# Kernel optimization log

Hardware: AMD Instinct MI355X
Metric: run time of the kernel (lower is better)

## Reference

```python
import jax, jax.numpy as jnp
import numpy as np

N = 100000           # nodes
E = 1600000          # edges (no self loops; added inside reference)
IN_DIM = 128
H1, C1 = 8, 16       # layer-1 heads, per-head channels (concat -> 128)
H2, C2 = 1, 40       # layer-2 heads, out channels (concat=False)


def setup_inputs() -> dict:
    key = jax.random.key(0)
    ks = jax.random.split(key, 10)
    x = jax.random.normal(ks[0], (N, IN_DIM), jnp.float32)
    src = jax.random.randint(ks[1], (E,), 0, N, dtype=jnp.int32)
    dst = jax.random.randint(ks[2], (E,), 0, N, dtype=jnp.int32)
    dst = jnp.where(dst == src, (dst + 1) % N, dst)  # emulate remove_self_loops
    edge_index = jnp.stack([src, dst], axis=0)
    sc = 0.05
    return {
        "x": x,
        "edge_index": edge_index,
        "W1": jax.random.normal(ks[3], (H1 * C1, IN_DIM), jnp.float32) * sc,
        "b1": jnp.zeros((H1 * C1,), jnp.float32),
        "att1": jax.random.normal(ks[4], (H1, 2 * C1), jnp.float32) * sc,
        "bias1": jnp.zeros((H1 * C1,), jnp.float32),
        "W2": jax.random.normal(ks[5], (H2 * C2, H1 * C1), jnp.float32) * sc,
        "b2": jnp.zeros((H2 * C2,), jnp.float32),
        "att2": jax.random.normal(ks[6], (H2, 2 * C2), jnp.float32) * sc,
        "bias2": jnp.zeros((C2,), jnp.float32),
    }


def _gat_layer(x, src, dst, W, b, att, bias, H, C, concat):
    n = x.shape[0]
    # add self loops (inputs are guaranteed self-loop free)
    loop = jnp.arange(n, dtype=src.dtype)
    s = jnp.concatenate([src, loop])
    d = jnp.concatenate([dst, loop])
    h = (x @ W.T + b).reshape(n, H, C)            # [N,H,C]
    # per-node halves of cat([x_i, x_j]) . att  -> gather scalars per edge
    a_i = jnp.einsum('nhc,hc->nh', h, att[:, :C])  # dst half
    a_j = jnp.einsum('nhc,hc->nh', h, att[:, C:])  # src half
    e = jax.nn.leaky_relu(a_i[d] + a_j[s], negative_slope=0.2)  # [Etot,H]
    # segment softmax over destination nodes (pyg_utils.softmax)
    m = jax.ops.segment_max(e, d, num_segments=n)
    ex = jnp.exp(e - m[d])
    denom = jax.ops.segment_sum(ex, d, num_segments=n)
    alpha = ex / (denom[d] + 1e-16)
    msg = h[s] * alpha[:, :, None]                # [Etot,H,C]
    out = jax.ops.segment_sum(msg.reshape(-1, H * C), d, num_segments=n)
    if not concat:
        out = out.reshape(n, H, C).mean(axis=1)
    return out + bias


def reference(x, edge_index, W1, b1, att1, bias1, W2, b2, att2, bias2):
    src, dst = edge_index[0], edge_index[1]
    h = _gat_layer(x, src, dst, W1, b1, att1, bias1, H1, C1, True)
    h = jax.nn.elu(h)  # dropout p=0 / eval -> no-op
    h = _gat_layer(h, src, dst, W2, b2, att2, bias2, H2, C2, False)
    return jax.nn.log_softmax(h, axis=1)
```

## Files before the change

### kernel.cpp

```cpp
#include <hip/hip_runtime.h>
#include <hip/hip_fp16.h>
#include <math.h>


typedef _Float16 f16x8 __attribute__((ext_vector_type(8)));
typedef float f32x4 __attribute__((ext_vector_type(4)));
typedef float f32x2 __attribute__((ext_vector_type(2)));

__device__ __forceinline__ float lrelu02(float x){ return x > 0.f ? x : 0.2f*x; }
__device__ __forceinline__ unsigned char f2fp8(float v){
  return (unsigned char)(__builtin_amdgcn_cvt_pk_fp8_f32(v, v, 0, false) & 0xff);
}

#define BSHIFT 8
#define BMASK  255
#define SPLIT_CHUNK 4096

__device__ __forceinline__ void split_body(int blk, const int* __restrict__ src,
    const int* __restrict__ dst, int* __restrict__ hp, int* __restrict__ tmp,
    int E, int nb1){
  __shared__ int hist[512];
  __shared__ int hoff[512];
  __shared__ int sb[256];
  int tid = threadIdx.x;
  #pragma unroll
  for (int t = tid; t < 512; t += 256) hist[t] = 0;
  __syncthreads();
  int lo = blk*SPLIT_CHUNK;
  int ds[16], ss[16];
  #pragma unroll
  for (int k = 0; k < 16; ++k){
    int i = lo + tid + k*256;
    bool p = i < E;
    ds[k] = p ? dst[i] : 0;
    ss[k] = p ? src[i] : 0;
    if (p) atomicAdd(&hist[ds[k] >> BSHIFT], 1);
  }
  __syncthreads();
  int v0 = hist[2*tid], v1 = hist[2*tid+1];
  sb[tid] = v0 + v1;
  __syncthreads();
  for (int off = 1; off < 256; off <<= 1){
    int x = (tid >= off) ? sb[tid-off] : 0;
    __syncthreads();
    sb[tid] += x;
    __syncthreads();
  }
  int base = (tid == 0) ? 0 : sb[tid-1];
  hoff[2*tid]   = base;
  hoff[2*tid+1] = base + v0;
  __syncthreads();
  for (int b = tid; b < nb1; b += 256) hp[blk*nb1 + b] = hoff[b];
  __syncthreads();
  #pragma unroll
  for (int k = 0; k < 16; ++k){
    int i = lo + tid + k*256;
    if (i < E){
      int r = atomicAdd(&hoff[ds[k] >> BSHIFT], 1);
      tmp[blk*SPLIT_CHUNK + r] = ss[k] | ((ds[k] & BMASK) << 17);
    }
  }
}

__device__ __forceinline__ void gemm1_body(int gb, const float* __restrict__ x,
    const _Float16* __restrict__ Wh, const _Float16* __restrict__ attB,
    const float* __restrict__ b1, const float* __restrict__ consts,
    unsigned char* __restrict__ h1f8, float* __restrict__ a1i, float* __restrict__ a1j, int N){
  int wid  = (gb*256 + (int)threadIdx.x) >> 6;
  int lane = threadIdx.x & 63;
  int m0 = wid*16;
  if (m0 >= N) return;
  int col = lane & 15, quad = lane >> 4;
  const float* xr = x + (size_t)(m0+col)*128 + quad*8;
  f32x4 acc[9];
  #pragma unroll
  for (int t=0;t<9;t++){ acc[t][0]=0.f; acc[t][1]=0.f; acc[t][2]=0.f; acc[t][3]=0.f; }
  #pragma unroll
  for (int q=0;q<4;q++){
    float4 f0 = ((const float4*)(xr + q*32))[0];
    float4 f1 = ((const float4*)(xr + q*32))[1];
    f16x8 a;
    a[0]=(_Float16)f0.x; a[1]=(_Float16)f0.y; a[2]=(_Float16)f0.z; a[3]=(_Float16)f0.w;
    a[4]=(_Float16)f1.x; a[5]=(_Float16)f1.y; a[6]=(_Float16)f1.z; a[7]=(_Float16)f1.w;
    #pragma unroll
    for (int t=0;t<8;t++){
      const f16x8* Bp = (const f16x8*)(Wh + (size_t)(t*16+col)*128 + q*32 + quad*8);
      acc[t] = __builtin_amdgcn_mfma_f32_16x16x32_f16(a, *Bp, acc[t], 0,0,0);
    }
    const f16x8* Ap = (const f16x8*)(attB + (size_t)col*128 + q*32 + quad*8);
    acc[8] = __builtin_amdgcn_mfma_f32_16x16x32_f16(a, *Ap, acc[8], 0,0,0);
  }
  #pragma unroll
  for (int t=0;t<8;t++){
    int c = t*16 + col;
    float bb = b1[c];
    #pragma unroll
    for (int r=0;r<4;r++){
      h1f8[(size_t)(m0 + quad*4 + r)*128 + c] = f2fp8(acc[t][r] + bb);
    }
  }
  float hb = consts[col];
  #pragma unroll
  for (int r=0;r<4;r++){
    int node = m0 + quad*4 + r;
    float v = acc[8][r] + hb;
    if (col < 8) a1i[node*8 + col] = v;
    else         a1j[node*8 + (col-8)] = v;
  }
}

__global__ __launch_bounds__(256) void k_fused1(const int* __restrict__ src,
    const int* __restrict__ dst, int* __restrict__ hp, int* __restrict__ tmp,
    int E, int nb1, int nchunk,
    const float* __restrict__ x, const _Float16* __restrict__ Wh,
    const _Float16* __restrict__ attB, const float* __restrict__ b1,
    const float* __restrict__ consts, unsigned char* __restrict__ h1f8,
    float* __restrict__ a1i, float* __restrict__ a1j, int N){
  if ((int)blockIdx.x < nchunk)
    split_body(blockIdx.x, src, dst, hp, tmp, E, nb1);
  else
    gemm1_body(blockIdx.x - nchunk, x, Wh, attB, b1, consts, h1f8, a1i, a1j, N);
}

__global__ __launch_bounds__(256) void k_colsum(const int* __restrict__ hp,
    int* __restrict__ tot, int nchunk, int nb1){
  __shared__ int red[256];
  int b = blockIdx.x;
  int t = threadIdx.x;
  int s = 0;
  for (int blk = t; blk < nchunk; blk += 256)
    s += hp[blk*nb1 + b + 1] - hp[blk*nb1 + b];
  red[t] = s;
  __syncthreads();
  for (int off = 128; off > 0; off >>= 1){
    if (t < off) red[t] += red[t+off];
    __syncthreads();
  }
  if (t == 0) tot[b] = red[0];
}

__global__ void k_bscan(const int* __restrict__ tot, int* __restrict__ bstart,
                        int* __restrict__ rowstart, int nbucket, int E, int N){
  __shared__ int lds[256];
  int t = threadIdx.x;
  int v[4]; int s = 0;
  #pragma unroll
  for (int k = 0; k < 4; ++k){
    int idx = t*4 + k;
    v[k] = (idx < nbucket) ? tot[idx] : 0;
    s += v[k];
  }
  lds[t] = s;
  __syncthreads();
  for (int off = 1; off < 256; off <<= 1){
    int x = (t >= off) ? lds[t-off] : 0;
    __syncthreads();
    lds[t] += x;
    __syncthreads();
  }
  int run = (t == 0) ? 0 : lds[t-1];
  #pragma unroll
  for (int k = 0; k < 4; ++k){
    int idx = t*4 + k;
    if (idx < nbucket) bstart[idx] = run;
    run += v[k];
  }
  if (t == 0){ bstart[nbucket] = E; rowstart[N] = E; }
}

#define STAGE_CAP 6144
__global__ __launch_bounds__(256) void k_final(const int* __restrict__ tmp,
    const int* __restrict__ hp, const int* __restrict__ bstart,
    int* __restrict__ rowstart, int* __restrict__ csr, int nchunk, int nb1, int N){
  __shared__ int stage[STAGE_CAP];
  __shared__ int c0[512];
  __shared__ int cv[512];
  __shared__ int ce[512];
  __shared__ int sb[256];
  __shared__ int h[256];
  __shared__ int sc[256];
  __shared__ int cur[256];
  int b = blockIdx.x;
  int tid = threadIdx.x;
  int base = bstart[b];
  int tot  = bstart[b+1] - base;
  #pragma unroll
  for (int t = tid; t < 512; t += 256){ c0[t] = 0; cv[t] = 0; }
  __syncthreads();
  for (int blk = tid; blk < nchunk; blk += 256){
    int o0 = hp[blk*nb1 + b];
    int o1 = hp[blk*nb1 + b + 1];
    c0[blk] = o0;
    cv[blk] = o1 - o0;
  }
  __syncthreads();
  int v0 = cv[2*tid], v1 = cv[2*tid+1];
  sb[tid] = v0 + v1;
  __syncthreads();
  for (int off = 1; off < 256; off <<= 1){
    int x = (tid >= off) ? sb[tid-off] : 0;
    __syncthreads();
    sb[tid] += x;
    __syncthreads();
  }
  int pbase = (tid == 0) ? 0 : sb[tid-1];
  ce[2*tid]   = pbase;
  ce[2*tid+1] = pbase + v0;
  __syncthreads();
  for (int blk = tid; blk < nchunk; blk += 256){
    int cnt = cv[blk];
    int out = ce[blk];
    const int* tb = tmp + blk*SPLIT_CHUNK + c0[blk];
    for (int j = 0; j < cnt; ++j){
      int o = out + j;
      if (o < STAGE_CAP) stage[o] = tb[j];
    }
  }
  if (tid < 256) h[tid] = 0;
  __syncthreads();
  if (tot > STAGE_CAP) tot = STAGE_CAP;
  for (int i = tid; i < tot; i += 256) atomicAdd(&h[stage[i] >> 17], 1);
  __syncthreads();
  sc[tid] = h[tid];
  __syncthreads();
  for (int off = 1; off < 256; off <<= 1){
    int x = (tid >= off) ? sc[tid-off] : 0;
    __syncthreads();
    sc[tid] += x;
    __syncthreads();
  }
  {
    int excl = sc[tid] - h[tid];
    int node = b*256 + tid;
    if (node < N) rowstart[node] = base + excl;
    cur[tid] = excl;
  }
  __syncthreads();
  for (int i = tid; i < tot; i += 256){
    int v = stage[i];
    int p = atomicAdd(&cur[v >> 17], 1);
    csr[base + p] = v & 0x1FFFF;
  }
}

__global__ void k_prep(const float* __restrict__ W1, const float* __restrict__ b1,
                       const float* __restrict__ att1,
                       const float* __restrict__ W2, const float* __restrict__ b2,
                       const float* __restrict__ att2,
                       _Float16* __restrict__ W1h, _Float16* __restrict__ W2h,
                       _Float16* __restrict__ attB1, _Float16* __restrict__ attB2,
                       float* __restrict__ consts){
  int i = blockIdx.x*blockDim.x + threadIdx.x;
  if (i < 16384){ W1h[i] = (_Float16)W1[i]; return; }
  i -= 16384;
  if (i < 6144){ int r = i >> 7; W2h[i] = (r < 40)? (_Float16)W2[i] : (_Float16)0.f; return; }
  i -= 6144;
  if (i < 2048){
    int j = i >> 7, k = i & 127;
    int h = j & 7, half = (j >> 3)*16;
    float s = 0.f;
    for (int c = 0; c < 16; ++c) s += att1[h*32 + half + c]*W1[(h*16+c)*128 + k];
    attB1[i] = (_Float16)s; return;
  }
  i -= 2048;
  if (i < 2048){
    int j = i >> 7, k = i & 127;
    float s = 0.f;
    if (j < 2){ const float* av = att2 + j*40; for (int c = 0; c < 40; ++c) s += av[c]*W2[c*128 + k]; }
    attB2[i] = (_Float16)s; return;
  }
  i -= 2048;
  if (i < 18){
    float s = 0.f;
    if (i < 8){ for (int c = 0; c < 16; ++c) s += b1[i*16+c]*att1[i*32+c]; }
    else if (i < 16){ int h = i-8; for (int c = 0; c < 16; ++c) s += b1[h*16+c]*att1[h*32+16+c]; }
    else if (i == 16){ for (int c = 0; c < 40; ++c) s += b2[c]*att2[c]; }
    else { for (int c = 0; c < 40; ++c) s += b2[c]*att2[40+c]; }
    consts[i] = s;
  }
}

__global__ __launch_bounds__(256) void k_agg1(const uint2* __restrict__ h1q,
    const float* __restrict__ a1i, const float* __restrict__ a1j,
    const int* __restrict__ rowstart, const int* __restrict__ csr,
    const float* __restrict__ bias, uint4* __restrict__ x2u4, int N){
  int lane = threadIdx.x & 63;
  int n = (blockIdx.x*blockDim.x + threadIdx.x) >> 6;
  if (n >= N) return;
  int ql = lane & 15, qt = lane >> 4;
  unsigned hd = (unsigned)ql >> 1;
  int rs = rowstart[n], re = rowstart[n+1];
  float ai2 = a1i[(unsigned)n*8u + hd];
  float a0=0.f,a1=0.f,a2=0.f,a3=0.f,a4=0.f,a5=0.f,a6=0.f,a7=0.f,den=0.f;
  {
    float w = (qt==0)? __expf(lrelu02(ai2 + a1j[(unsigned)n*8u + hd])) : 0.f;
    uint2 u = h1q[(unsigned)n*16u + (unsigned)ql];
    f32x2 f0 = __builtin_amdgcn_cvt_pk_f32_fp8((int)u.x, false);
    f32x2 f1 = __builtin_amdgcn_cvt_pk_f32_fp8((int)u.x, true);
    f32x2 f2 = __builtin_amdgcn_cvt_pk_f32_fp8((int)u.y, false);
    f32x2 f3 = __builtin_amdgcn_cvt_pk_f32_fp8((int)u.y, true);
    a0=w*f0[0]; a1=w*f0[1]; a2=w*f1[0]; a3=w*f1[1];
    a4=w*f2[0]; a5=w*f2[1]; a6=w*f3[0]; a7=w*f3[1];
    den = w;
  }
  int last = re - 1;
  if (rs < re){
    unsigned cs0 = (unsigned)csr[min(rs+ 0+qt,last)];
    unsigned cs1 = (unsigned)csr[min(rs+ 4+qt,last)];
    unsigned cs2 = (unsigned)csr[min(rs+ 8+qt,last)];
    unsigned cs3 = (unsigned)csr[min(rs+12+qt,last)];
    unsigned cs4 = (unsigned)csr[min(rs+16+qt,last)];
    unsigned cs5 = (unsigned)csr[min(rs+20+qt,last)];
    unsigned cs6 = (unsigned)csr[min(rs+24+qt,last)];
    unsigned cs7 = (unsigned)csr[min(rs+28+qt,last)];
    float aj0 = a1j[cs0*8u+hd], aj1 = a1j[cs1*8u+hd];
    float aj2 = a1j[cs2*8u+hd], aj3 = a1j[cs3*8u+hd];
    float aj4 = a1j[cs4*8u+hd], aj5 = a1j[cs5*8u+hd];
    float aj6 = a1j[cs6*8u+hd], aj7 = a1j[cs7*8u+hd];
    uint2 u0 = h1q[(size_t)cs0*16u + (unsigned)ql];
    uint2 u1 = h1q[(size_t)cs1*16u + (unsigned)ql];
    uint2 u2 = h1q[(size_t)cs2*16u + (unsigned)ql];
    uint2 u3 = h1q[(size_t)cs3*16u + (unsigned)ql];
    int e0 = rs;

#define AGG1_ST(US, CF, CS, AJ, OFF)                                         \
    {                                                                        \
      uint2 cur = US;                                                        \
      US = h1q[(size_t)CF*16u + (unsigned)ql];                               \
      unsigned nc = (unsigned)csr[min(e0+OFF+32+qt, last)];                  \
      float w = (e0+OFF+qt < re)? __expf(lrelu02(ai2 + AJ)) : 0.f;           \
      den += w;                                                              \
      f32x2 g0 = __builtin_amdgcn_cvt_pk_f32_fp8((int)cur.x, false);         \
      f32x2 g1 = __builtin_amdgcn_cvt_pk_f32_fp8((int)cur.x, true);          \
      f32x2 g2 = __builtin_amdgcn_cvt_pk_f32_fp8((int)cur.y, false);         \
      f32x2 g3 = __builtin_amdgcn_cvt_pk_f32_fp8((int)cur.y, true);          \
      a0 += w*g0[0]; a1 += w*g0[1]; a2 += w*g1[0]; a3 += w*g1[1];            \
      a4 += w*g2[0]; a5 += w*g2[1]; a6 += w*g3[0]; a7 += w*g3[1];            \
      CS = nc; AJ = a1j[nc*8u + hd];                                         \
    }

    while (e0 < re){
      AGG1_ST(u0, cs4, cs0, aj0, 0)
      if (e0+4 >= re) break;
      AGG1_ST(u1, cs5, cs1, aj1, 4)
      if (e0+8 >= re) break;
      AGG1_ST(u2, cs6, cs2, aj2, 8)
      if (e0+12 >= re) break;
      AGG1_ST(u3, cs7, cs3, aj3, 12)
      if (e0+16 >= re) break;
      AGG1_ST(u0, cs0, cs4, aj4, 16)
      if (e0+20 >= re) break;
      AGG1_ST(u1, cs1, cs5, aj5, 20)
      if (e0+24 >= re) break;
      AGG1_ST(u2, cs2, cs6, aj6, 24)
      if (e0+28 >= re) break;
      AGG1_ST(u3, cs3, cs7, aj7, 28)
      e0 += 32;
    }
#undef AGG1_ST
  }
  #pragma unroll
  for (int off = 16; off < 64; off <<= 1){
    den += __shfl_xor(den, off);
    a0 += __shfl_xor(a0, off); a1 += __shfl_xor(a1, off);
    a2 += __shfl_xor(a2, off); a3 += __shfl_xor(a3, off);
    a4 += __shfl_xor(a4, off); a5 += __shfl_xor(a5, off);
    a6 += __shfl_xor(a6, off); a7 += __shfl_xor(a7, off);
  }
  if (qt == 0){
    float invd = 1.f/(den + 1e-16f);
    const float4* b4 = (const float4*)(bias + 8*ql);
    float4 bl = b4[0], bh = b4[1];
    float o0=a0*invd+bl.x, o1=a1*invd+bl.y, o2=a2*invd+bl.z, o3=a3*invd+bl.w;
    float o4=a4*invd+bh.x, o5=a5*invd+bh.y, o6=a6*invd+bh.z, o7=a7*invd+bh.w;
    o0=(o0>0.f)?o0:(__expf(o0)-1.f); o1=(o1>0.f)?o1:(__expf(o1)-1.f);
    o2=(o2>0.f)?o2:(__expf(o2)-1.f); o3=(o3>0.f)?o3:(__expf(o3)-1.f);
    o4=(o4>0.f)?o4:(__expf(o4)-1.f); o5=(o5>0.f)?o5:(__expf(o5)-1.f);
    o6=(o6>0.f)?o6:(__expf(o6)-1.f); o7=(o7>0.f)?o7:(__expf(o7)-1.f);
    __half2 p0 = __floats2half2_rn(o0,o1), p1 = __floats2half2_rn(o2,o3);
    __half2 p2 = __floats2half2_rn(o4,o5), p3 = __floats2half2_rn(o6,o7);
    uint4 o;
    o.x = *(unsigned*)&p0; o.y = *(unsigned*)&p1; o.z = *(unsigned*)&p2; o.w = *(unsigned*)&p3;
    x2u4[(unsigned)n*16u + (unsigned)ql] = o;
  }
}

__global__ __launch_bounds__(256) void k_gemm2(const _Float16* __restrict__ xh,
    const _Float16* __restrict__ Wh, const _Float16* __restrict__ attB,
    const float* __restrict__ b2, const float* __restrict__ consts,
    unsigned char* __restrict__ h2f8, float* __restrict__ a2i, float* __restrict__ a2j, int N){
  int wid  = (blockIdx.x*256 + threadIdx.x) >> 6;
  int lane = threadIdx.x & 63;
  int m0 = wid*16;
  if (m0 >= N) return;
  int col = lane & 15, quad = lane >> 4;
  const f16x8* A8 = (const f16x8*)(xh + (size_t)(m0+col)*128 + quad*8);
  f32x4 acc[4];
  #pragma unroll
  for (int t=0;t<4;t++){ acc[t][0]=0.f; acc[t][1]=0.f; acc[t][2]=0.f; acc[t][3]=0.f; }
  #pragma unroll
  for (int q=0;q<4;q++){
    f16x8 a = A8[q*4];
    #pragma unroll
    for (int t=0;t<3;t++){
      const f16x8* Bp = (const f16x8*)(Wh + (size_t)(t*16+col)*128 + q*32 + quad*8);
      acc[t] = __builtin_amdgcn_mfma_f32_16x16x32_f16(a, *Bp, acc[t], 0,0,0);
    }
    const f16x8* Bp2 = (const f16x8*)(attB + (size_t)col*128 + q*32 + quad*8);
    acc[3] = __builtin_amdgcn_mfma_f32_16x16x32_f16(a, *Bp2, acc[3], 0,0,0);
  }
  #pragma unroll
  for (int t=0;t<3;t++){
    int c = t*16 + col;
    if (c < 40){
      float bb = b2[c];
      #pragma unroll
      for (int r=0;r<4;r++){
        h2f8[(size_t)(m0 + quad*4 + r)*40 + c] = f2fp8(acc[t][r] + bb);
      }
    }
  }
  if (col < 2){
    float cc = consts[16 + col];
    #pragma unroll
    for (int r=0;r<4;r++){
      int node = m0 + quad*4 + r;
      if (col == 0) a2i[node] = acc[3][r] + cc;
      else          a2j[node] = acc[3][r] + cc;
    }
  }
}

__global__ __launch_bounds__(256) void k_agg2(const unsigned* __restrict__ h2u,
    const float* __restrict__ a2i, const float* __restrict__ a2j,
    const int* __restrict__ rowstart, const int* __restrict__ csr,
    const float* __restrict__ bias, float* __restrict__ out, int N){
  int lane = threadIdx.x & 63;
  int wid = (blockIdx.x*blockDim.x + threadIdx.x) >> 6;
  int qt = lane >> 4, ql = lane & 15;
  int n = wid*4 + qt;
  if (n >= N) return;
  bool act = ql < 10;
  unsigned cl = act ? (unsigned)ql : 0u;
  int rs = rowstart[n], re = rowstart[n+1];
  float ai = a2i[n];
  float wself = __expf(lrelu02(ai + a2j[n]));
  float a0,a1,a2,a3,den;
  {
    unsigned u = h2u[(unsigned)n*10u + cl];
    f32x2 f0 = __builtin_amdgcn_cvt_pk_f32_fp8((int)u, false);
    f32x2 f1 = __builtin_amdgcn_cvt_pk_f32_fp8((int)u, true);
    a0 = wself*f0[0]; a1 = wself*f0[1]; a2 = wself*f1[0]; a3 = wself*f1[1];
    den = wself;
  }
  if (rs < re){
    int last = re - 1;
    unsigned cs0 = (unsigned)csr[min(rs+0,last)];
    unsigned cs1 = (unsigned)csr[min(rs+1,last)];
    unsigned cs2 = (unsigned)csr[min(rs+2,last)];
    unsigned cs3 = (unsigned)csr[min(rs+3,last)];
    unsigned cs4 = (unsigned)csr[min(rs+4,last)];
    unsigned cs5 = (unsigned)csr[min(rs+5,last)];
    unsigned cs6 = (unsigned)csr[min(rs+6,last)];
    unsigned cs7 = (unsigned)csr[min(rs+7,last)];
    float aj0 = a2j[cs0], aj1 = a2j[cs1], aj2 = a2j[cs2], aj3 = a2j[cs3];
    float aj4 = a2j[cs4], aj5 = a2j[cs5], aj6 = a2j[cs6], aj7 = a2j[cs7];
    unsigned u0 = h2u[cs0*10u + cl];
    unsigned u1 = h2u[cs1*10u + cl];
    unsigned u2 = h2u[cs2*10u + cl];
    unsigned u3 = h2u[cs3*10u + cl];
    int e0 = rs;

#define AGG2_ST(US, CF, CS, AJ, OFF)                                         \
    {                                                                        \
      unsigned cur = US;                                                     \
      US = h2u[CF*10u + cl];                                                 \
      unsigned nc = (unsigned)csr[min(e0+OFF+8, last)];                      \
      float w = (e0+OFF < re)? __expf(lrelu02(ai + AJ)) : 0.f;               \
      den += w;                                                              \
      f32x2 g0 = __builtin_amdgcn_cvt_pk_f32_fp8((int)cur, false);           \
      f32x2 g1 = __builtin_amdgcn_cvt_pk_f32_fp8((int)cur, true);            \
      a0 += w*g0[0]; a1 += w*g0[1]; a2 += w*g1[0]; a3 += w*g1[1];            \
      CS = nc; AJ = a2j[nc];                                                 \
    }

    while (e0 < re){
      AGG2_ST(u0, cs4, cs0, aj0, 0)
      AGG2_ST(u1, cs5, cs1, aj1, 1)
      AGG2_ST(u2, cs6, cs2, aj2, 2)
      AGG2_ST(u3, cs7, cs3, aj3, 3)
      AGG2_ST(u0, cs0, cs4, aj4, 4)
      AGG2_ST(u1, cs1, cs5, aj5, 5)
      AGG2_ST(u2, cs2, cs6, aj6, 6)
      AGG2_ST(u3, cs3, cs7, aj7, 7)
      e0 += 8;
    }
#undef AGG2_ST
  }
  float invd = 1.f/(den + 1e-16f);
  const float4* b4 = (const float4*)(bias + 4*cl);
  float4 bb = b4[0];
  float v0 = a0*invd + bb.x, v1 = a1*invd + bb.y;
  float v2 = a2*invd + bb.z, v3 = a3*invd + bb.w;
  float mv = act ? fmaxf(fmaxf(v0,v1), fmaxf(v2,v3)) : -INFINITY;
  #pragma unroll
  for (int off = 1; off < 16; off <<= 1) mv = fmaxf(mv, __shfl_xor(mv, off));
  float se = act ? (__expf(v0-mv)+__expf(v1-mv)+__expf(v2-mv)+__expf(v3-mv)) : 0.f;
  #pragma unroll
  for (int off = 1; off < 16; off <<= 1) se += __shfl_xor(se, off);
  float ls = __logf(se);
  if (act){
    float4 o = make_float4(v0-mv-ls, v1-mv-ls, v2-mv-ls, v3-mv-ls);
    ((float4*)out)[(unsigned)n*10u + cl] = o;
  }
}

extern "C" void kernel_launch(void* const* d_in, const int* in_sizes, int n_in,
                              void* d_out, int out_size, void* d_ws, size_t ws_size,
                              hipStream_t stream){
  const float* x     = (const float*)d_in[0];
  const int*   ei    = (const int*)  d_in[1];
  const float* W1    = (const float*)d_in[2];
  const float* b1    = (const float*)d_in[3];
  const float* att1  = (const float*)d_in[4];
  const float* bias1 = (const float*)d_in[5];
  const float* W2    = (const float*)d_in[6];
  const float* b2    = (const float*)d_in[7];
  const float* att2  = (const float*)d_in[8];
  const float* bias2 = (const float*)d_in[9];
  int N = in_sizes[0] / 128;
  int E = in_sizes[1] / 2;
  const int* src = ei;
  const int* dst = ei + E;

  char* ws = (char*)d_ws;
  size_t off = 0;
  auto alloc = [&](size_t bytes)->char*{
    char* p = ws + off; off += (bytes + 255) & ~(size_t)255; return p;
  };
  unsigned char* h1f8 = (unsigned char*)alloc((size_t)N*128);
  _Float16*      x2h  = (_Float16*)alloc((size_t)N*128*2);
  unsigned char* h2f8 = (unsigned char*)alloc((size_t)N*40);
  float* a1i  = (float*)alloc((size_t)N*8*4);
  float* a1j  = (float*)alloc((size_t)N*8*4);
  float* a2i  = (float*)alloc((size_t)N*4);
  float* a2j  = (float*)alloc((size_t)N*4);
  _Float16* W1h   = (_Float16*)alloc(16384*2);
  _Float16* W2h   = (_Float16*)alloc(6144*2);
  _Float16* attB1 = (_Float16*)alloc(2048*2);
  _Float16* attB2 = (_Float16*)alloc(2048*2);
  float* consts = (float*)alloc(18*4);
  int*   rowst = (int*)  alloc((size_t)(N+1)*4);
  int*   csr   = (int*)  alloc((size_t)E*4);

  int nbucket = (N + BMASK) >> BSHIFT;
  int nb1 = nbucket + 1;
  int nchunk = (E + SPLIT_CHUNK - 1)/SPLIT_CHUNK;

  int*   hp     = (int*)alloc((size_t)nchunk*nb1*4);
  int*   tot    = (int*)alloc((size_t)nbucket*4);
  int*   bstart = (int*)alloc((size_t)(nbucket+1)*4);
  int*   tmp    = (int*)x2h;

  int gblk = ((N+15)/16 + 3)/4;

  k_prep<<<105, 256, 0, stream>>>(W1, b1, att1, W2, b2, att2, W1h, W2h, attB1, attB2, consts);
  k_fused1<<<nchunk + gblk, 256, 0, stream>>>(src, dst, hp, tmp, E, nb1, nchunk,
                                              x, W1h, attB1, b1, consts, h1f8, a1i, a1j, N);
  k_colsum<<<nbucket, 256, 0, stream>>>(hp, tot, nchunk, nb1);
  k_bscan<<<1, 256, 0, stream>>>(tot, bstart, rowst, nbucket, E, N);
  k_final<<<nbucket, 256, 0, stream>>>(tmp, hp, bstart, rowst, csr, nchunk, nb1, N);

  k_agg1<<<(N*64+255)/256, 256, 0, stream>>>((const uint2*)h1f8, a1i, a1j, rowst, csr, bias1, (uint4*)x2h, N);

  k_gemm2<<<gblk, 256, 0, stream>>>(x2h, W2h, attB2, b2, consts, h2f8, a2i, a2j, N);
  k_agg2<<<(N+15)/16, 256, 0, stream>>>((const unsigned*)h2f8, a2i, a2j, rowst, csr, bias2, (float*)d_out, N);
}
```

Baseline: 290.9 us.

## Fuse layer-2 GEMM into layer-1 aggregation via shared-memory tile

The layer-1 aggregation kernel now runs 16 waves per 1024-thread block, one node per wave, and stages the ELU'd fp16 outputs in shared memory. After a barrier, four waves run the layer-2 MFMA projection and attention dot products directly from that tile. This drops the separate GEMM launch and the round trip of the N×128 fp16 intermediate through global memory. In exchange it adds a block-wide sync that makes fast waves wait on the slowest-degree node, uses large blocks that may limit occupancy, and gives the temp buffer its own allocation.

```diff
diff --git a/kernel.cpp b/kernel.cpp
--- a/kernel.cpp
+++ b/kernel.cpp
@@ -280,153 +280,153 @@
   }
 }
 
-__global__ __launch_bounds__(256) void k_agg1(const uint2* __restrict__ h1q,
+__global__ __launch_bounds__(1024) void k_agg1(const uint2* __restrict__ h1q,
     const float* __restrict__ a1i, const float* __restrict__ a1j,
     const int* __restrict__ rowstart, const int* __restrict__ csr,
-    const float* __restrict__ bias, uint4* __restrict__ x2u4, int N){
-  int lane = threadIdx.x & 63;
-  int n = (blockIdx.x*blockDim.x + threadIdx.x) >> 6;
-  if (n >= N) return;
+    const float* __restrict__ bias,
+    const _Float16* __restrict__ W2h, const _Float16* __restrict__ attB2,
+    const float* __restrict__ b2, const float* __restrict__ consts,
+    unsigned char* __restrict__ h2f8, float* __restrict__ a2i, float* __restrict__ a2j,
+    int N){
+  __shared__ uint4 xt4[16][16];
+  int tid = threadIdx.x;
+  int w = tid >> 6, lane = tid & 63;
+  int m0 = blockIdx.x*16;
+  int n = m0 + w;
   int ql = lane & 15, qt = lane >> 4;
-  unsigned hd = (unsigned)ql >> 1;
-  int rs = rowstart[n], re = rowstart[n+1];
-  float ai2 = a1i[(unsigned)n*8u + hd];
-  float a0=0.f,a1=0.f,a2=0.f,a3=0.f,a4=0.f,a5=0.f,a6=0.f,a7=0.f,den=0.f;
-  {
-    float w = (qt==0)? __expf(lrelu02(ai2 + a1j[(unsigned)n*8u + hd])) : 0.f;
-    uint2 u = h1q[(unsigned)n*16u + (unsigned)ql];
-    f32x2 f0 = __builtin_amdgcn_cvt_pk_f32_fp8((int)u.x, false);
-    f32x2 f1 = __builtin_amdgcn_cvt_pk_f32_fp8((int)u.x, true);
-    f32x2 f2 = __builtin_amdgcn_cvt_pk_f32_fp8((int)u.y, false);
-    f32x2 f3 = __builtin_amdgcn_cvt_pk_f32_fp8((int)u.y, true);
-    a0=w*f0[0]; a1=w*f0[1]; a2=w*f1[0]; a3=w*f1[1];
-    a4=w*f2[0]; a5=w*f2[1]; a6=w*f3[0]; a7=w*f3[1];
-    den = w;
-  }
-  int last = re - 1;
-  if (rs < re){
-    unsigned cs0 = (unsigned)csr[min(rs+ 0+qt,last)];
-    unsigned cs1 = (unsigned)csr[min(rs+ 4+qt,last)];
-    unsigned cs2 = (unsigned)csr[min(rs+ 8+qt,last)];
-    unsigned cs3 = (unsigned)csr[min(rs+12+qt,last)];
-    unsigned cs4 = (unsigned)csr[min(rs+16+qt,last)];
-    unsigned cs5 = (unsigned)csr[min(rs+20+qt,last)];
-    unsigned cs6 = (unsigned)csr[min(rs+24+qt,last)];
-    unsigned cs7 = (unsigned)csr[min(rs+28+qt,last)];
-    float aj0 = a1j[cs0*8u+hd], aj1 = a1j[cs1*8u+hd];
-    float aj2 = a1j[cs2*8u+hd], aj3 = a1j[cs3*8u+hd];
-    float aj4 = a1j[cs4*8u+hd], aj5 = a1j[cs5*8u+hd];
-    float aj6 = a1j[cs6*8u+hd], aj7 = a1j[cs7*8u+hd];
-    uint2 u0 = h1q[(size_t)cs0*16u + (unsigned)ql];
-    uint2 u1 = h1q[(size_t)cs1*16u + (unsigned)ql];
-    uint2 u2 = h1q[(size_t)cs2*16u + (unsigned)ql];
-    uint2 u3 = h1q[(size_t)cs3*16u + (unsigned)ql];
-    int e0 = rs;
+
+  if (n < N){
+    unsigned hd = (unsigned)ql >> 1;
+    int rs = rowstart[n], re = rowstart[n+1];
+    float ai2 = a1i[(unsigned)n*8u + hd];
+    float a0=0.f,a1=0.f,a2=0.f,a3=0.f,a4=0.f,a5=0.f,a6=0.f,a7=0.f,den=0.f;
+    {
+      float wg = (qt==0)? __expf(lrelu02(ai2 + a1j[(unsigned)n*8u + hd])) : 0.f;
+      uint2 u = h1q[(unsigned)n*16u + (unsigned)ql];
+      f32x2 f0 = __builtin_amdgcn_cvt_pk_f32_fp8((int)u.x, false);
+      f32x2 f1 = __builtin_amdgcn_cvt_pk_f32_fp8((int)u.x, true);
+      f32x2 f2 = __builtin_amdgcn_cvt_pk_f32_fp8((int)u.y, false);
+      f32x2 f3 = __builtin_amdgcn_cvt_pk_f32_fp8((int)u.y, true);
+      a0=wg*f0[0]; a1=wg*f0[1]; a2=wg*f1[0]; a3=wg*f1[1];
+      a4=wg*f2[0]; a5=wg*f2[1]; a6=wg*f3[0]; a7=wg*f3[1];
+      den = wg;
+    }
+    int last = re - 1;
+    if (rs < re){
+      unsigned cs0 = (unsigned)csr[min(rs+ 0+qt,last)];
+      unsigned cs1 = (unsigned)csr[min(rs+ 4+qt,last)];
+      unsigned cs2 = (unsigned)csr[min(rs+ 8+qt,last)];
+      unsigned cs3 = (unsigned)csr[min(rs+12+qt,last)];
+      unsigned cs4 = (unsigned)csr[min(rs+16+qt,last)];
+      unsigned cs5 = (unsigned)csr[min(rs+20+qt,last)];
+      unsigned cs6 = (unsigned)csr[min(rs+24+qt,last)];
+      unsigned cs7 = (unsigned)csr[min(rs+28+qt,last)];
+      float aj0 = a1j[cs0*8u+hd], aj1 = a1j[cs1*8u+hd];
+      float aj2 = a1j[cs2*8u+hd], aj3 = a1j[cs3*8u+hd];
+      float aj4 = a1j[cs4*8u+hd], aj5 = a1j[cs5*8u+hd];
+      float aj6 = a1j[cs6*8u+hd], aj7 = a1j[cs7*8u+hd];
+      uint2 u0 = h1q[(size_t)cs0*16u + (unsigned)ql];
+      uint2 u1 = h1q[(size_t)cs1*16u + (unsigned)ql];
+      uint2 u2 = h1q[(size_t)cs2*16u + (unsigned)ql];
+      uint2 u3 = h1q[(size_t)cs3*16u + (unsigned)ql];
+      int e0 = rs;
 
 #define AGG1_ST(US, CF, CS, AJ, OFF)                                         \
-    {                                                                        \
-      uint2 cur = US;                                                        \
-      US = h1q[(size_t)CF*16u + (unsigned)ql];                               \
-      unsigned nc = (unsigned)csr[min(e0+OFF+32+qt, last)];                  \
-      float w = (e0+OFF+qt < re)? __expf(lrelu02(ai2 + AJ)) : 0.f;           \
-      den += w;                                                              \
-      f32x2 g0 = __builtin_amdgcn_cvt_pk_f32_fp8((int)cur.x, false);         \
-      f32x2 g1 = __builtin_amdgcn_cvt_pk_f32_fp8((int)cur.x, true);          \
-      f32x2 g2 = __builtin_amdgcn_cvt_pk_f32_fp8((int)cur.y, false);         \
-      f32x2 g3 = __builtin_amdgcn_cvt_pk_f32_fp8((int)cur.y, true);          \
-      a0 += w*g0[0]; a1 += w*g0[1]; a2 += w*g1[0]; a3 += w*g1[1];            \
-      a4 += w*g2[0]; a5 += w*g2[1]; a6 += w*g3[0]; a7 += w*g3[1];            \
-      CS = nc; AJ = a1j[nc*8u + hd];                                         \
-    }
-
-    while (e0 < re){
-      AGG1_ST(u0, cs4, cs0, aj0, 0)
-      if (e0+4 >= re) break;
-      AGG1_ST(u1, cs5, cs1, aj1, 4)
-      if (e0+8 >= re) break;
-      AGG1_ST(u2, cs6, cs2, aj2, 8)
-      if (e0+12 >= re) break;
-      AGG1_ST(u3, cs7, cs3, aj3, 12)
-      if (e0+16 >= re) break;
-      AGG1_ST(u0, cs0, cs4, aj4, 16)
-      if (e0+20 >= re) break;
-      AGG1_ST(u1, cs1, cs5, aj5, 20)
-      if (e0+24 >= re) break;
-      AGG1_ST(u2, cs2, cs6, aj6, 24)
-      if (e0+28 >= re) break;
-      AGG1_ST(u3, cs3, cs7, aj7, 28)
-      e0 += 32;
-    }
+      {                                                                      \
+        uint2 cur = US;                                                      \
+        US = h1q[(size_t)CF*16u + (unsigned)ql];                             \
+        unsigned nc = (unsigned)csr[min(e0+OFF+32+qt, last)];                \
+        float wg = (e0+OFF+qt < re)? __expf(lrelu02(ai2 + AJ)) : 0.f;        \
+        den += wg;                                                           \
+        f32x2 g0 = __builtin_amdgcn_cvt_pk_f32_fp8((int)cur.x, false);       \
+        f32x2 g1 = __builtin_amdgcn_cvt_pk_f32_fp8((int)cur.x, true);        \
+        f32x2 g2 = __builtin_amdgcn_cvt_pk_f32_fp8((int)cur.y, false);       \
+        f32x2 g3 = __builtin_amdgcn_cvt_pk_f32_fp8((int)cur.y, true);        \
+        a0 += wg*g0[0]; a1 += wg*g0[1]; a2 += wg*g1[0]; a3 += wg*g1[1];      \
+        a4 += wg*g2[0]; a5 += wg*g2[1]; a6 += wg*g3[0]; a7 += wg*g3[1];      \
+        CS = nc; AJ = a1j[nc*8u + hd];                                       \
+      }
+
+      while (e0 < re){
+        AGG1_ST(u0, cs4, cs0, aj0, 0)
+        if (e0+4 >= re) break;
+        AGG1_ST(u1, cs5, cs1, aj1, 4)
+        if (e0+8 >= re) break;
+        AGG1_ST(u2, cs6, cs2, aj2, 8)
+        if (e0+12 >= re) break;
+        AGG1_ST(u3, cs7, cs3, aj3, 12)
+        if (e0+16 >= re) break;
+        AGG1_ST(u0, cs0, cs4, aj4, 16)
+        if (e0+20 >= re) break;
+        AGG1_ST(u1, cs1, cs5, aj5, 20)
+        if (e0+24 >= re) break;
+        AGG1_ST(u2, cs2, cs6, aj6, 24)
+        if (e0+28 >= re) break;
+        AGG1_ST(u3, cs3, cs7, aj7, 28)
+        e0 += 32;
+      }
 #undef AGG1_ST
-  }
-  #pragma unroll
-  for (int off = 16; off < 64; off <<= 1){
-    den += __shfl_xor(den, off);
-    a0 += __shfl_xor(a0, off); a1 += __shfl_xor(a1, off);
-    a2 += __shfl_xor(a2, off); a3 += __shfl_xor(a3, off);
-    a4 += __shfl_xor(a4, off); a5 += __shfl_xor(a5, off);
-    a6 += __shfl_xor(a6, off); a7 += __shfl_xor(a7, off);
-  }
-  if (qt == 0){
-    float invd = 1.f/(den + 1e-16f);
-    const float4* b4 = (const float4*)(bias + 8*ql);
-    float4 bl = b4[0], bh = b4[1];
-    float o0=a0*invd+bl.x, o1=a1*invd+bl.y, o2=a2*invd+bl.z, o3=a3*invd+bl.w;
-    float o4=a4*invd+bh.x, o5=a5*invd+bh.y, o6=a6*invd+bh.z, o7=a7*invd+bh.w;
-    o0=(o0>0.f)?o0:(__expf(o0)-1.f); o1=(o1>0.f)?o1:(__expf(o1)-1.f);
-    o2=(o2>0.f)?o2:(__expf(o2)-1.f); o3=(o3>0.f)?o3:(__expf(o3)-1.f);
-    o4=(o4>0.f)?o4:(__expf(o4)-1.f); o5=(o5>0.f)?o5:(__expf(o5)-1.f);
-    o6=(o6>0.f)?o6:(__expf(o6)-1.f); o7=(o7>0.f)?o7:(__expf(o7)-1.f);
-    __half2 p0 = __floats2half2_rn(o0,o1), p1 = __floats2half2_rn(o2,o3);
-    __half2 p2 = __floats2half2_rn(o4,o5), p3 = __floats2half2_rn(o6,o7);
-    uint4 o;
-    o.x = *(unsigned*)&p0; o.y = *(unsigned*)&p1; o.z = *(unsigned*)&p2; o.w = *(unsigned*)&p3;
-    x2u4[(unsigned)n*16u + (unsigned)ql] = o;
-  }
-}
-
-__global__ __launch_bounds__(256) void k_gemm2(const _Float16* __restrict__ xh,
-    const _Float16* __restrict__ Wh, const _Float16* __restrict__ attB,
-    const float* __restrict__ b2, const float* __restrict__ consts,
-    unsigned char* __restrict__ h2f8, float* __restrict__ a2i, float* __restrict__ a2j, int N){
-  int wid  = (blockIdx.x*256 + threadIdx.x) >> 6;
-  int lane = threadIdx.x & 63;
-  int m0 = wid*16;
-  if (m0 >= N) return;
-  int col = lane & 15, quad = lane >> 4;
-  const f16x8* A8 = (const f16x8*)(xh + (size_t)(m0+col)*128 + quad*8);
-  f32x4 acc[4];
-  #pragma unroll
-  for (int t=0;t<4;t++){ acc[t][0]=0.f; acc[t][1]=0.f; acc[t][2]=0.f; acc[t][3]=0.f; }
-  #pragma unroll
-  for (int q=0;q<4;q++){
-    f16x8 a = A8[q*4];
+    }
     #pragma unroll
-    for (int t=0;t<3;t++){
-      const f16x8* Bp = (const f16x8*)(Wh + (size_t)(t*16+col)*128 + q*32 + quad*8);
-      acc[t] = __builtin_amdgcn_mfma_f32_16x16x32_f16(a, *Bp, acc[t], 0,0,0);
-    }
-    const f16x8* Bp2 = (const f16x8*)(attB + (size_t)col*128 + q*32 + quad*8);
-    acc[3] = __builtin_amdgcn_mfma_f32_16x16x32_f16(a, *Bp2, acc[3], 0,0,0);
-  }
-  #pragma unroll
-  for (int t=0;t<3;t++){
-    int c = t*16 + col;
-    if (c < 40){
-      float bb = b2[c];
-      #pragma unroll
-      for (int r=0;r<4;r++){
-        h2f8[(size_t)(m0 + quad*4 + r)*40 + c] = f2fp8(acc[t][r] + bb);
+    for (int off = 16; off < 64; off <<= 1){
+      den += __shfl_xor(den, off);
+      a0 += __shfl_xor(a0, off); a1 += __shfl_xor(a1, off);
+      a2 += __shfl_xor(a2, off); a3 += __shfl_xor(a3, off);
+      a4 += __shfl_xor(a4, off); a5 += __shfl_xor(a5, off);
+      a6 += __shfl_xor(a6, off); a7 += __shfl_xor(a7, off);
+    }
+    if (qt == 0){
+      float invd = 1.f/(den + 1e-16f);
+      const float4* b4 = (const float4*)(bias + 8*ql);
+      float4 bl = b4[0], bh = b4[1];
+      float o0=a0*invd+bl.x, o1=a1*invd+bl.y, o2=a2*invd+bl.z, o3=a3*invd+bl.w;
+      float o4=a4*invd+bh.x, o5=a5*invd+bh.y, o6=a6*invd+bh.z, o7=a7*invd+bh.w;
+      o0=(o0>0.f)?o0:(__expf(o0)-1.f); o1=(o1>0.f)?o1:(__expf(o1)-1.f);
+      o2=(o2>0.f)?o2:(__expf(o2)-1.f); o3=(o3>0.f)?o3:(__expf(o3)-1.f);
+      o4=(o4>0.f)?o4:(__expf(o4)-1.f); o5=(o5>0.f)?o5:(__expf(o5)-1.f);
+      o6=(o6>0.f)?o6:(__expf(o6)-1.f); o7=(o7>0.f)?o7:(__expf(o7)-1.f);
+      __half2 p0 = __floats2half2_rn(o0,o1), p1 = __floats2half2_rn(o2,o3);
+      __half2 p2 = __floats2half2_rn(o4,o5), p3 = __floats2half2_rn(o6,o7);
+      uint4 o;
+      o.x = *(unsigned*)&p0; o.y = *(unsigned*)&p1; o.z = *(unsigned*)&p2; o.w = *(unsigned*)&p3;
+      xt4[w][ql] = o;
+    }
+  }
+  __syncthreads();
+  if (w < 4){
+    int col = lane & 15, quad = lane >> 4;
+    const _Float16* xrow = (const _Float16*)&xt4[col][0];
+    f32x4 acc; acc[0]=0.f; acc[1]=0.f; acc[2]=0.f; acc[3]=0.f;
+    #pragma unroll
+    for (int q=0;q<4;q++){
+      f16x8 a = *(const f16x8*)(xrow + q*32 + quad*8);
+      const f16x8* Bp = (w < 3)
+        ? (const f16x8*)(W2h  + (size_t)(w*16+col)*128 + q*32 + quad*8)
+        : (const f16x8*)(attB2 + (size_t)col*128       + q*32 + quad*8);
+      acc = __builtin_amdgcn_mfma_f32_16x16x32_f16(a, *Bp, acc, 0,0,0);
+    }
+    if (w < 3){
+      int c = w*16 + col;
+      if (c < 40){
+        float bb = b2[c];
+        #pragma unroll
+        for (int r=0;r<4;r++){
+          int node = m0 + quad*4 + r;
+          if (node < N) h2f8[(size_t)node*40 + c] = f2fp8(acc[r] + bb);
+        }
       }
-    }
-  }
-  if (col < 2){
-    float cc = consts[16 + col];
-    #pragma unroll
-    for (int r=0;r<4;r++){
-      int node = m0 + quad*4 + r;
-      if (col == 0) a2i[node] = acc[3][r] + cc;
-      else          a2j[node] = acc[3][r] + cc;
+    } else {
+      if (col < 2){
+        float cc = consts[16 + col];
+        #pragma unroll
+        for (int r=0;r<4;r++){
+          int node = m0 + quad*4 + r;
+          if (node < N){
+            if (col == 0) a2i[node] = acc[r] + cc;
+            else          a2j[node] = acc[r] + cc;
+          }
+        }
+      }
     }
   }
 }
@@ -476,11 +476,11 @@
       unsigned cur = US;                                                     \
       US = h2u[CF*10u + cl];                                                 \
       unsigned nc = (unsigned)csr[min(e0+OFF+8, last)];                      \
-      float w = (e0+OFF < re)? __expf(lrelu02(ai + AJ)) : 0.f;               \
-      den += w;                                                              \
+      float wg = (e0+OFF < re)? __expf(lrelu02(ai + AJ)) : 0.f;              \
+      den += wg;                                                             \
       f32x2 g0 = __builtin_amdgcn_cvt_pk_f32_fp8((int)cur, false);           \
       f32x2 g1 = __builtin_amdgcn_cvt_pk_f32_fp8((int)cur, true);            \
-      a0 += w*g0[0]; a1 += w*g0[1]; a2 += w*g1[0]; a3 += w*g1[1];            \
+      a0 += wg*g0[0]; a1 += wg*g0[1]; a2 += wg*g1[0]; a3 += wg*g1[1];        \
       CS = nc; AJ = a2j[nc];                                                 \
     }
 
@@ -539,7 +539,6 @@
     char* p = ws + off; off += (bytes + 255) & ~(size_t)255; return p;
   };
   unsigned char* h1f8 = (unsigned char*)alloc((size_t)N*128);
-  _Float16*      x2h  = (_Float16*)alloc((size_t)N*128*2);
   unsigned char* h2f8 = (unsigned char*)alloc((size_t)N*40);
   float* a1i  = (float*)alloc((size_t)N*8*4);
   float* a1j  = (float*)alloc((size_t)N*8*4);
@@ -560,7 +559,7 @@
   int*   hp     = (int*)alloc((size_t)nchunk*nb1*4);
   int*   tot    = (int*)alloc((size_t)nbucket*4);
   int*   bstart = (int*)alloc((size_t)(nbucket+1)*4);
-  int*   tmp    = (int*)x2h;
+  int*   tmp    = (int*)alloc((size_t)nchunk*SPLIT_CHUNK*4);
 
   int gblk = ((N+15)/16 + 3)/4;
 
@@ -571,8 +570,8 @@
   k_bscan<<<1, 256, 0, stream>>>(tot, bstart, rowst, nbucket, E, N);
   k_final<<<nbucket, 256, 0, stream>>>(tmp, hp, bstart, rowst, csr, nchunk, nb1, N);
 
-  k_agg1<<<(N*64+255)/256, 256, 0, stream>>>((const uint2*)h1f8, a1i, a1j, rowst, csr, bias1, (uint4*)x2h, N);
-
-  k_gemm2<<<gblk, 256, 0, stream>>>(x2h, W2h, attB2, b2, consts, h2f8, a2i, a2j, N);
+  k_agg1<<<(N+15)/16, 1024, 0, stream>>>((const uint2*)h1f8, a1i, a1j, rowst, csr, bias1,
+                                         W2h, attB2, b2, consts, h2f8, a2i, a2j, N);
+
   k_agg2<<<(N+15)/16, 256, 0, stream>>>((const unsigned*)h2f8, a2i, a2j, rowst, csr, bias2, (float*)d_out, N);
 }
```

New measurement: 300.7 us. +3.4%, slower.

## Split agg1 in halves and overlap second half with gemm2 on first half

Applied to the files above, without the earlier changes.

Layer-1 aggregation is split into two node ranges. The second range runs in one fused launch whose blocks also do the layer-2 GEMM for the first range, which that range's aggregation has already produced. A final small GEMM launch covers the remaining nodes. The goal is to overlap the memory-bound gather with the MFMA GEMM and shorten the serial agg1→gemm2 chain, at the cost of one extra launch and a heterogeneous fused kernel whose register use is set by the larger of the two paths.

```diff
diff --git a/kernel.cpp b/kernel.cpp
--- a/kernel.cpp
+++ b/kernel.cpp
@@ -280,13 +280,12 @@
   }
 }
 
-__global__ __launch_bounds__(256) void k_agg1(const uint2* __restrict__ h1q,
+__device__ __forceinline__ void agg1_node(int n, const uint2* __restrict__ h1q,
     const float* __restrict__ a1i, const float* __restrict__ a1j,
     const int* __restrict__ rowstart, const int* __restrict__ csr,
     const float* __restrict__ bias, uint4* __restrict__ x2u4, int N){
+  if (n >= N) return;
   int lane = threadIdx.x & 63;
-  int n = (blockIdx.x*blockDim.x + threadIdx.x) >> 6;
-  if (n >= N) return;
   int ql = lane & 15, qt = lane >> 4;
   unsigned hd = (unsigned)ql >> 1;
   int rs = rowstart[n], re = rowstart[n+1];
@@ -385,14 +384,12 @@
   }
 }
 
-__global__ __launch_bounds__(256) void k_gemm2(const _Float16* __restrict__ xh,
+__device__ __forceinline__ void gemm2_tile(int m0, const _Float16* __restrict__ xh,
     const _Float16* __restrict__ Wh, const _Float16* __restrict__ attB,
     const float* __restrict__ b2, const float* __restrict__ consts,
     unsigned char* __restrict__ h2f8, float* __restrict__ a2i, float* __restrict__ a2j, int N){
-  int wid  = (blockIdx.x*256 + threadIdx.x) >> 6;
+  if (m0 >= N) return;
   int lane = threadIdx.x & 63;
-  int m0 = wid*16;
-  if (m0 >= N) return;
   int col = lane & 15, quad = lane >> 4;
   const f16x8* A8 = (const f16x8*)(xh + (size_t)(m0+col)*128 + quad*8);
   f32x4 acc[4];
@@ -429,6 +426,41 @@
       else          a2j[node] = acc[3][r] + cc;
     }
   }
+}
+
+__global__ __launch_bounds__(256) void k_agg1(const uint2* __restrict__ h1q,
+    const float* __restrict__ a1i, const float* __restrict__ a1j,
+    const int* __restrict__ rowstart, const int* __restrict__ csr,
+    const float* __restrict__ bias, uint4* __restrict__ x2u4, int n0, int N){
+  int n = n0 + ((blockIdx.x*256 + (int)threadIdx.x) >> 6);
+  agg1_node(n, h1q, a1i, a1j, rowstart, csr, bias, x2u4, N);
+}
+
+__global__ __launch_bounds__(256) void k_fused2(const uint2* __restrict__ h1q,
+    const float* __restrict__ a1i, const float* __restrict__ a1j,
+    const int* __restrict__ rowstart, const int* __restrict__ csr,
+    const float* __restrict__ bias, uint4* __restrict__ x2u4,
+    const _Float16* __restrict__ xh, const _Float16* __restrict__ W2h,
+    const _Float16* __restrict__ attB2, const float* __restrict__ b2,
+    const float* __restrict__ consts, unsigned char* __restrict__ h2f8,
+    float* __restrict__ a2i, float* __restrict__ a2j,
+    int aggB, int H, int N){
+  if ((int)blockIdx.x < aggB){
+    int n = H + ((blockIdx.x*256 + (int)threadIdx.x) >> 6);
+    agg1_node(n, h1q, a1i, a1j, rowstart, csr, bias, x2u4, N);
+  } else {
+    int m0 = (((blockIdx.x - aggB)*256 + (int)threadIdx.x) >> 6)*16;
+    gemm2_tile(m0, xh, W2h, attB2, b2, consts, h2f8, a2i, a2j, N);
+  }
+}
+
+__global__ __launch_bounds__(256) void k_gemm2(const _Float16* __restrict__ xh,
+    const _Float16* __restrict__ Wh, const _Float16* __restrict__ attB,
+    const float* __restrict__ b2, const float* __restrict__ consts,
+    unsigned char* __restrict__ h2f8, float* __restrict__ a2i, float* __restrict__ a2j,
+    int nb, int N){
+  int m0 = nb + (((blockIdx.x*256 + (int)threadIdx.x) >> 6)*16);
+  gemm2_tile(m0, xh, Wh, attB, b2, consts, h2f8, a2i, a2j, N);
 }
 
 __global__ __launch_bounds__(256) void k_agg2(const unsigned* __restrict__ h2u,
@@ -476,11 +508,11 @@
       unsigned cur = US;                                                     \
       US = h2u[CF*10u + cl];                                                 \
       unsigned nc = (unsigned)csr[min(e0+OFF+8, last)];                      \
-      float w = (e0+OFF < re)? __expf(lrelu02(ai + AJ)) : 0.f;               \
-      den += w;                                                              \
+      float wg = (e0+OFF < re)? __expf(lrelu02(ai + AJ)) : 0.f;              \
+      den += wg;                                                             \
       f32x2 g0 = __builtin_amdgcn_cvt_pk_f32_fp8((int)cur, false);           \
       f32x2 g1 = __builtin_amdgcn_cvt_pk_f32_fp8((int)cur, true);            \
-      a0 += w*g0[0]; a1 += w*g0[1]; a2 += w*g1[0]; a3 += w*g1[1];            \
+      a0 += wg*g0[0]; a1 += wg*g0[1]; a2 += wg*g1[0]; a3 += wg*g1[1];        \
       CS = nc; AJ = a2j[nc];                                                 \
     }
 
@@ -571,8 +603,17 @@
   k_bscan<<<1, 256, 0, stream>>>(tot, bstart, rowst, nbucket, E, N);
   k_final<<<nbucket, 256, 0, stream>>>(tmp, hp, bstart, rowst, csr, nchunk, nb1, N);
 
-  k_agg1<<<(N*64+255)/256, 256, 0, stream>>>((const uint2*)h1f8, a1i, a1j, rowst, csr, bias1, (uint4*)x2h, N);
-
-  k_gemm2<<<gblk, 256, 0, stream>>>(x2h, W2h, attB2, b2, consts, h2f8, a2i, a2j, N);
+  int H = ((N/2)/64)*64;
+  if (H > 0)
+    k_agg1<<<H/4, 256, 0, stream>>>((const uint2*)h1f8, a1i, a1j, rowst, csr, bias1,
+                                    (uint4*)x2h, 0, N);
+  int aggB = (N - H + 3)/4;
+  int g2A  = H/64;
+  k_fused2<<<aggB + g2A, 256, 0, stream>>>((const uint2*)h1f8, a1i, a1j, rowst, csr, bias1,
+                                           (uint4*)x2h, x2h, W2h, attB2, b2, consts,
+                                           h2f8, a2i, a2j, aggB, H, N);
+  k_gemm2<<<(N - H + 63)/64, 256, 0, stream>>>(x2h, W2h, attB2, b2, consts,
+                                               h2f8, a2i, a2j, H, N);
+
   k_agg2<<<(N+15)/16, 256, 0, stream>>>((const unsigned*)h2f8, a2i, a2j, rowst, csr, bias2, (float*)d_out, N);
 }
```

Result: slower. 306.4 us (+5.3%).
